# Kernel optimization log

Measured on AMD Instinct MI355X. Metric: run time of the kernel, lower is better.

## Reference

```python
import jax, jax.numpy as jnp
import numpy as np

B, NQ, NK, D_IN, HD = 1, 16384, 7933, 1024, 512
R = 0.3  # keep-top-r fraction used for the quantile threshold


def _l2norm(x):
    # matches F.normalize(p=2, dim=-1, eps=1e-12)
    n = jnp.linalg.norm(x, axis=-1, keepdims=True)
    return x / jnp.maximum(n, 1e-12)


def setup_inputs() -> dict:
    key = jax.random.key(0)
    ks = jax.random.split(key, 10)
    s = 0.02
    return {
        "query": jax.random.normal(ks[0], (B, NQ, D_IN), jnp.float32),
        "key_x": jax.random.normal(ks[1], (B, NK, D_IN), jnp.float32),
        "wq_w": jax.random.normal(ks[2], (HD, D_IN), jnp.float32) * s,
        "wq_b": jnp.zeros((HD,), jnp.float32),
        "wk_w": jax.random.normal(ks[3], (HD, D_IN), jnp.float32) * s,
        "wk_b": jnp.zeros((HD,), jnp.float32),
        "wa_w": jax.random.normal(ks[4], (1, NK), jnp.float32) * s,
        "wa_b": jnp.zeros((1,), jnp.float32),
        "cls_w": jax.random.normal(ks[5], (1, HD), jnp.float32) * s,
        "cls_b": jnp.zeros((1,), jnp.float32),
    }


def reference(query, key_x, wq_w, wq_b, wk_w, wk_b, wa_w, wa_b, cls_w, cls_b):
    # WQ / WK: Linear + Tanh
    q = jnp.tanh(jnp.einsum("bnd,hd->bnh", query, wq_w) + wq_b)   # [B,NQ,HD]
    k = jnp.tanh(jnp.einsum("bnd,hd->bnh", key_x, wk_w) + wk_b)   # [B,NK,HD]
    # normalized dot-product scores
    A = jnp.einsum("bqh,bkh->bqk", _l2norm(q), _l2norm(k))        # [B,NQ,NK]
    # WA: Linear(NK -> 1)
    A1 = jnp.einsum("bqk,ok->bqo", A, wa_w) + wa_b                # [B,NQ,1]
    # quantile threshold from batch 0 (torch: sorted ascending, index -int(r*NQ))
    thre = jax.lax.stop_gradient(jnp.sort(A1[0, :, 0])[-int(R * NQ)])
    A1 = jnp.where(A1 > thre, A1, 0.0)                            # F.threshold(., thre, 0)
    attn = jax.nn.softmax(A1, axis=1)                             # softmax over NQ (zeros included)
    attn_t = jnp.transpose(attn, (0, 2, 1))                       # [B,1,NQ]
    z = jnp.matmul(attn_t, q).reshape(-1, HD)                     # [B,HD]
    y_prob = z @ cls_w.T + cls_b                                  # [B,1]
    return (y_prob, attn_t)
```

## Files before the change

kernel.cpp:

```cpp
#include <hip/hip_runtime.h>
#include <math.h>

#define NQ 16384
#define NK 7933
#define DI 1024
#define HD 512
#define RANK_TARGET 11469

typedef __bf16 bf16x8 __attribute__((ext_vector_type(8)));
typedef float  f32x4  __attribute__((ext_vector_type(4)));

#define GLOAD_LDS16(g, l)                                                     \
  __builtin_amdgcn_global_load_lds(                                           \
      (const __attribute__((address_space(1))) void*)(g),                     \
      (__attribute__((address_space(3))) void*)(l), 16, 0, 0)

__device__ __forceinline__ unsigned mapf(float f) {
  unsigned b = __float_as_uint(f);
  return (b & 0x80000000u) ? ~b : (b | 0x80000000u);
}

__device__ __forceinline__ bf16x8 cvt8(float4 a, float4 b) {
  bf16x8 o;
  o[0] = (__bf16)a.x; o[1] = (__bf16)a.y; o[2] = (__bf16)a.z; o[3] = (__bf16)a.w;
  o[4] = (__bf16)b.x; o[5] = (__bf16)b.y; o[6] = (__bf16)b.z; o[7] = (__bf16)b.w;
  return o;
}

__global__ void conv_wk(const float* __restrict__ wq, const float* __restrict__ wk,
                        const float* __restrict__ key,
                        __bf16* __restrict__ wqbf, __bf16* __restrict__ wkbf,
                        __bf16* __restrict__ kbf, unsigned* __restrict__ zero_region) {
  if (blockIdx.x == 0) {
    for (int j = threadIdx.x; j < 1088; j += 256) zero_region[j] = 0u;
  }
  const int NK8 = NK * DI / 8;
  const int W8  = HD * DI / 8;
  const int total = NK8 + 2 * W8;
  int i = blockIdx.x * blockDim.x + threadIdx.x;
  int stride = gridDim.x * blockDim.x;
  for (; i < total; i += stride) {
    const float* s; __bf16* d; int j;
    if (i < NK8)            { s = key; d = kbf;  j = i; }
    else if (i < NK8 + W8)  { s = wq;  d = wqbf; j = i - NK8; }
    else                    { s = wk;  d = wkbf; j = i - NK8 - W8; }
    float4 a = ((const float4*)s)[2 * j];
    float4 b = ((const float4*)s)[2 * j + 1];
    ((bf16x8*)d)[j] = cvt8(a, b);
  }
}

__global__ __launch_bounds__(512, 4)
void mega_gemms(const __bf16* __restrict__ kbf, const __bf16* __restrict__ wkbf,
                const float* __restrict__ wk_b, const float* __restrict__ wa,
                float* __restrict__ v,
                const float* __restrict__ query, const __bf16* __restrict__ wqbf,
                const float* __restrict__ wq_b, float* __restrict__ qtanh) {
  __shared__ __align__(16) char smem[81920];
  const int bid = blockIdx.x;
  const int tid = threadIdx.x;
  const int lane = tid & 63;
  const int wave = tid >> 6;
  const int srow = lane >> 3;
  const int scol = ((lane & 7) ^ srow) << 3;
  const int lrow = lane & 15;
  const int chi  = lane >> 4;
  constexpr int K = DI;

  if (bid < 124) {
    __bf16* sA = (__bf16*)smem;
    __bf16* sB = (__bf16*)(smem + 16384);
    float* ssrow = (float*)smem;
    const int m0 = bid * 64;

    int gaA = m0 + wave * 8 + srow; if (gaA > NK - 1) gaA = NK - 1;
    const __bf16* Ap = kbf + (size_t)gaA * K + scol;
    const __bf16* Bp[8];
#pragma unroll
    for (int c = 0; c < 8; ++c)
      Bp[c] = wkbf + (size_t)(wave * 64 + c * 8 + srow) * K + scol;

    f32x4 acc[4][4] = {};

    GLOAD_LDS16(Ap, &sA[wave * 512]);
#pragma unroll
    for (int c = 0; c < 8; ++c)
      GLOAD_LDS16(Bp[c], &sB[(wave * 8 + c) * 512]);
    __syncthreads();

    int buf = 0;
    for (int t = 0; t < 16; ++t) {
      const int kk = t * 64;
      if (t < 15)
        GLOAD_LDS16(Ap + kk + 64, &sA[(buf ^ 1) * 4096 + wave * 512]);
      const __bf16* sAc = sA + buf * 4096;
#pragma unroll
      for (int ks = 0; ks < 64; ks += 32) {
        const int cc = (ks >> 3) + chi;
        const int sw = ((cc ^ (lrow & 7)) << 3);
        bf16x8 af[4], bfr[4];
#pragma unroll
        for (int mi = 0; mi < 4; ++mi)
          af[mi] = *(const bf16x8*)(&sAc[(mi * 16 + lrow) * 64 + sw]);
#pragma unroll
        for (int ni = 0; ni < 4; ++ni)
          bfr[ni] = *(const bf16x8*)(&sB[(wave * 64 + ni * 16 + lrow) * 64 + sw]);
#pragma unroll
        for (int mi = 0; mi < 4; ++mi)
#pragma unroll
          for (int ni = 0; ni < 4; ++ni)
            acc[mi][ni] = __builtin_amdgcn_mfma_f32_16x16x32_bf16(af[mi], bfr[ni], acc[mi][ni], 0, 0, 0);
      }
      if (t < 15) {
        __syncthreads();
#pragma unroll
        for (int c = 0; c < 8; ++c)
          GLOAD_LDS16(Bp[c] + kk + 64, &sB[(wave * 8 + c) * 512]);
        __syncthreads();
        buf ^= 1;
      }
    }

    __syncthreads();
    if (tid < 64) ssrow[tid] = 0.f;
    __syncthreads();

    float b4[4];
#pragma unroll
    for (int ni = 0; ni < 4; ++ni) b4[ni] = wk_b[wave * 64 + ni * 16 + lrow];

#pragma unroll
    for (int mi = 0; mi < 4; ++mi)
#pragma unroll
      for (int ni = 0; ni < 4; ++ni)
#pragma unroll
        for (int r = 0; r < 4; ++r)
          acc[mi][ni][r] = tanhf(acc[mi][ni][r] + b4[ni]);

#pragma unroll
    for (int mi = 0; mi < 4; ++mi)
#pragma unroll
      for (int r = 0; r < 4; ++r) {
        float ps = 0.f;
#pragma unroll
        for (int ni = 0; ni < 4; ++ni) ps += acc[mi][ni][r] * acc[mi][ni][r];
#pragma unroll
        for (int off = 1; off < 16; off <<= 1) ps += __shfl_xor(ps, off);
        if ((lane & 15) == 0)
          atomicAdd(&ssrow[mi * 16 + (lane >> 4) * 4 + r], ps);
      }
    __syncthreads();

    if (tid < 64) {
      int grow = m0 + tid;
      float s = 0.f;
      if (grow < NK) s = wa[grow] / fmaxf(sqrtf(ssrow[tid]), 1e-12f);
      ssrow[tid] = s;
    }
    __syncthreads();

    float sc[4][4];
#pragma unroll
    for (int mi = 0; mi < 4; ++mi)
#pragma unroll
      for (int r = 0; r < 4; ++r)
        sc[mi][r] = ssrow[mi * 16 + (lane >> 4) * 4 + r];

#pragma unroll
    for (int ni = 0; ni < 4; ++ni) {
      float cs = 0.f;
#pragma unroll
      for (int mi = 0; mi < 4; ++mi)
#pragma unroll
        for (int r = 0; r < 4; ++r)
          cs += acc[mi][ni][r] * sc[mi][r];
      cs += __shfl_xor(cs, 16);
      cs += __shfl_xor(cs, 32);
      if (lane < 16) atomicAdd(&v[wave * 64 + ni * 16 + lane], cs);
    }
  } else {
    __bf16* sA = (__bf16*)smem;
    __bf16* sB = (__bf16*)(smem + 16384);
    const int qi = bid - 124;
    const int m0 = (qi >> 1) * 64;
    const int n0 = (qi & 1) * 256;
    const int wr = wave >> 2;
    const int wc = wave & 3;

    const int arow = tid >> 3;
    const int acb  = tid & 7;
    const int aoff = arow * 64 + ((acb ^ (arow & 7)) << 3);
    const float* ap = query + (size_t)(m0 + arow) * K + acb * 8;

    const __bf16* Bp0 = wqbf + (size_t)(n0 + (wave * 4 + 0) * 8 + srow) * K + scol;
    const __bf16* Bp1 = wqbf + (size_t)(n0 + (wave * 4 + 1) * 8 + srow) * K + scol;
    const __bf16* Bp2 = wqbf + (size_t)(n0 + (wave * 4 + 2) * 8 + srow) * K + scol;
    const __bf16* Bp3 = wqbf + (size_t)(n0 + (wave * 4 + 3) * 8 + srow) * K + scol;

    f32x4 acc[2][4] = {};

    {
      float4 x0 = *(const float4*)(ap);
      float4 x1 = *(const float4*)(ap + 4);
      GLOAD_LDS16(Bp0, &sB[(wave * 4 + 0) * 512]);
      GLOAD_LDS16(Bp1, &sB[(wave * 4 + 1) * 512]);
      GLOAD_LDS16(Bp2, &sB[(wave * 4 + 2) * 512]);
      GLOAD_LDS16(Bp3, &sB[(wave * 4 + 3) * 512]);
      *(bf16x8*)&sA[aoff] = cvt8(x0, x1);
      __syncthreads();
    }

    int buf = 0;
    for (int t = 0; t < 16; ++t) {
      const int kk = t * 64;
      float4 x0, x1;
      if (t < 15) {
        x0 = *(const float4*)(ap + kk + 64);
        x1 = *(const float4*)(ap + kk + 68);
        const int ob = buf ^ 1;
        GLOAD_LDS16(Bp0 + kk + 64, &sB[ob * 16384 + (wave * 4 + 0) * 512]);
        GLOAD_LDS16(Bp1 + kk + 64, &sB[ob * 16384 + (wave * 4 + 1) * 512]);
        GLOAD_LDS16(Bp2 + kk + 64, &sB[ob * 16384 + (wave * 4 + 2) * 512]);
        GLOAD_LDS16(Bp3 + kk + 64, &sB[ob * 16384 + (wave * 4 + 3) * 512]);
      }
      const __bf16* sAc = sA + buf * 4096;
      const __bf16* sBc = sB + buf * 16384;
#pragma unroll
      for (int ks = 0; ks < 64; ks += 32) {
        const int cc = (ks >> 3) + chi;
        const int sw = ((cc ^ (lrow & 7)) << 3);
        bf16x8 af[2], bfr[4];
        af[0] = *(const bf16x8*)(&sAc[(wr * 32 + lrow) * 64 + sw]);
        af[1] = *(const bf16x8*)(&sAc[(wr * 32 + 16 + lrow) * 64 + sw]);
#pragma unroll
        for (int ni = 0; ni < 4; ++ni)
          bfr[ni] = *(const bf16x8*)(&sBc[(wc * 64 + ni * 16 + lrow) * 64 + sw]);
#pragma unroll
        for (int ni = 0; ni < 4; ++ni) {
          acc[0][ni] = __builtin_amdgcn_mfma_f32_16x16x32_bf16(af[0], bfr[ni], acc[0][ni], 0, 0, 0);
          acc[1][ni] = __builtin_amdgcn_mfma_f32_16x16x32_bf16(af[1], bfr[ni], acc[1][ni], 0, 0, 0);
        }
      }
      if (t < 15) {
        *(bf16x8*)&sA[(buf ^ 1) * 4096 + aoff] = cvt8(x0, x1);
        __syncthreads();
        buf ^= 1;
      }
    }

    const int rbase = m0 + wr * 32 + ((lane >> 4) << 2);
    const int cbase = n0 + wc * 64 + (lane & 15);
    float b4[4];
#pragma unroll
    for (int ni = 0; ni < 4; ++ni) b4[ni] = wq_b[cbase + ni * 16];
#pragma unroll
    for (int mi = 0; mi < 2; ++mi)
#pragma unroll
      for (int r = 0; r < 4; ++r) {
        int grow = rbase + mi * 16 + r;
#pragma unroll
        for (int ni = 0; ni < 4; ++ni)
          qtanh[(size_t)grow * HD + cbase + ni * 16] =
              tanhf(acc[mi][ni][r] + b4[ni]);
      }
  }
}

__global__ __launch_bounds__(256)
void a1_pass(const float* __restrict__ qt, const float* __restrict__ v,
             const float* __restrict__ wa_b, float* __restrict__ A1) {
  const int tid = threadIdx.x, lane = tid & 63, wave = tid >> 6;
  const float wab = wa_b[0];
  const float4* vp = (const float4*)(v + lane * 8);
  float4 vv0 = vp[0], vv1 = vp[1];
  const int gw = blockIdx.x * 4 + wave;
  for (int r = gw; r < NQ; r += 2048) {
    const float4* p = (const float4*)(qt + (size_t)r * HD + lane * 8);
    float4 u = p[0], w = p[1];
    float dot = u.x * vv0.x + u.y * vv0.y + u.z * vv0.z + u.w * vv0.w
              + w.x * vv1.x + w.y * vv1.y + w.z * vv1.z + w.w * vv1.w;
    float ss  = u.x * u.x + u.y * u.y + u.z * u.z + u.w * u.w
              + w.x * w.x + w.y * w.y + w.z * w.z + w.w * w.w;
#pragma unroll
    for (int off = 32; off; off >>= 1) {
      dot += __shfl_xor(dot, off);
      ss  += __shfl_xor(ss, off);
    }
    if (lane == 0) A1[r] = dot / fmaxf(sqrtf(ss), 1e-12f) + wab;
  }
}

__global__ __launch_bounds__(1024)
void select_kernel(const float* __restrict__ A1, float* __restrict__ scf) {
  __shared__ unsigned wred1[16], wred2[16], wred3[16];
  __shared__ unsigned s_res;
  const int t = threadIdx.x, lane = t & 63, wave = t >> 6;
  unsigned kloc[16];
#pragma unroll 4
  for (int j = 0; j < 16; ++j) kloc[j] = mapf(A1[j * 1024 + t]);
  if (t == 0) s_res = 0u;
  __syncthreads();

  for (int b = 30; b >= 0; b -= 2) {
    const unsigned res = s_res;
    const unsigned t1 = res | (1u << b);
    const unsigned t2 = res | (2u << b);
    const unsigned t3 = res | (3u << b);
    unsigned c1 = 0, c2 = 0, c3 = 0;
#pragma unroll
    for (int j = 0; j < 16; ++j) {
      unsigned k = kloc[j];
      c1 += (k < t1); c2 += (k < t2); c3 += (k < t3);
    }
#pragma unroll
    for (int off = 32; off; off >>= 1) {
      c1 += __shfl_xor(c1, off);
      c2 += __shfl_xor(c2, off);
      c3 += __shfl_xor(c3, off);
    }
    if (lane == 0) { wred1[wave] = c1; wred2[wave] = c2; wred3[wave] = c3; }
    __syncthreads();
    if (t == 0) {
      unsigned C1 = 0, C2 = 0, C3 = 0;
      for (int w = 0; w < 16; ++w) { C1 += wred1[w]; C2 += wred2[w]; C3 += wred3[w]; }
      unsigned nr = res;
      if (C3 <= RANK_TARGET)      nr = t3;
      else if (C2 <= RANK_TARGET) nr = t2;
      else if (C1 <= RANK_TARGET) nr = t1;
      s_res = nr;
    }
    __syncthreads();
  }
  if (t == 0) {
    unsigned key = s_res;
    unsigned bits = (key & 0x80000000u) ? (key ^ 0x80000000u) : ~key;
    scf[0] = __uint_as_float(bits);
  }
}

__global__ __launch_bounds__(256)
void expz(const float* __restrict__ A1, const float* __restrict__ qt,
          float* __restrict__ scf, float* __restrict__ e_out,
          float* __restrict__ z) {
  __shared__ float vpart[4][512];
  __shared__ float esum[4];
  const int tid = threadIdx.x, lane = tid & 63, wave = tid >> 6;
  const float thre = scf[0];
  const int gw = blockIdx.x * 4 + wave;
  const int tw = gridDim.x * 4;
  float acc[8] = {0, 0, 0, 0, 0, 0, 0, 0};
  float es = 0.f;
  for (int r = gw; r < NQ; r += tw) {
    float x = A1[r]; x = (x > thre) ? x : 0.f;
    float e = expf(x - thre);
    if (lane == 0) e_out[r] = e;
    es += e;
    const float4* p = (const float4*)(qt + (size_t)r * HD + lane * 8);
    float4 u = p[0], w = p[1];
    acc[0] += e * u.x; acc[1] += e * u.y; acc[2] += e * u.z; acc[3] += e * u.w;
    acc[4] += e * w.x; acc[5] += e * w.y; acc[6] += e * w.z; acc[7] += e * w.w;
  }
  if (lane == 0) esum[wave] = es;
#pragma unroll
  for (int j = 0; j < 8; ++j) vpart[wave][lane * 8 + j] = acc[j];
  __syncthreads();
  for (int c = tid; c < 512; c += 256)
    atomicAdd(&z[c], vpart[0][c] + vpart[1][c] + vpart[2][c] + vpart[3][c]);
  if (tid == 0) atomicAdd(&scf[2], esum[0] + esum[1] + esum[2] + esum[3]);
}

__global__ __launch_bounds__(256)
void finalize(float* __restrict__ attn, const float* __restrict__ scf,
              const float* __restrict__ z, const float* __restrict__ cls_w,
              const float* __restrict__ cls_b, float* __restrict__ y) {
  const float invZ = 1.f / scf[2];
  if (blockIdx.x < 64) {
    int i = blockIdx.x * 256 + threadIdx.x;
    attn[i] *= invZ;
  } else if (threadIdx.x < 64) {
    const int lane = threadIdx.x;
    const float4* zp = (const float4*)(z + lane * 8);
    const float4* wp = (const float4*)(cls_w + lane * 8);
    float4 a = zp[0], b = zp[1], c = wp[0], d = wp[1];
    float dot = a.x * c.x + a.y * c.y + a.z * c.z + a.w * c.w
              + b.x * d.x + b.y * d.y + b.z * d.z + b.w * d.w;
#pragma unroll
    for (int off = 32; off; off >>= 1) dot += __shfl_xor(dot, off);
    if (lane == 0) y[0] = dot * invZ + cls_b[0];
  }
}

#define OFF_WQBF 0u
#define OFF_WKBF 1048576u
#define OFF_KBF  2097152u
#define OFF_QT   18874368u
#define OFF_A1   52428800u
#define OFF_V    52494336u
#define OFF_Z    52496384u
#define OFF_SC   52498432u

extern "C" void kernel_launch(void* const* d_in, const int* in_sizes, int n_in,
                              void* d_out, int out_size, void* d_ws, size_t ws_size,
                              hipStream_t stream) {
  const float* query = (const float*)d_in[0];
  const float* key_x = (const float*)d_in[1];
  const float* wq_w  = (const float*)d_in[2];
  const float* wq_b  = (const float*)d_in[3];
  const float* wk_w  = (const float*)d_in[4];
  const float* wk_b  = (const float*)d_in[5];
  const float* wa_w  = (const float*)d_in[6];
  const float* wa_b  = (const float*)d_in[7];
  const float* cls_w = (const float*)d_in[8];
  const float* cls_b = (const float*)d_in[9];
  float* out = (float*)d_out;

  char* ws = (char*)d_ws;
  __bf16* wqbf  = (__bf16*)(ws + OFF_WQBF);
  __bf16* wkbf  = (__bf16*)(ws + OFF_WKBF);
  __bf16* kbf   = (__bf16*)(ws + OFF_KBF);
  float*  qtanh = (float*)(ws + OFF_QT);
  float*  A1    = (float*)(ws + OFF_A1);
  float*  v     = (float*)(ws + OFF_V);
  float*  z     = (float*)(ws + OFF_Z);
  float*  scf   = (float*)(ws + OFF_SC);
  float*  out_attn = out + 1;

  conv_wk<<<2048, 256, 0, stream>>>(wq_w, wk_w, key_x, wqbf, wkbf, kbf,
                                    (unsigned*)v);

  mega_gemms<<<636, 512, 0, stream>>>(kbf, wkbf, wk_b, wa_w, v,
                                      query, wqbf, wq_b, qtanh);

  a1_pass<<<512, 256, 0, stream>>>(qtanh, v, wa_b, A1);

  select_kernel<<<1, 1024, 0, stream>>>(A1, scf);

  expz<<<256, 256, 0, stream>>>(A1, qtanh, scf, out_attn, z);

  finalize<<<65, 256, 0, stream>>>(out_attn, scf, z, cls_w, cls_b, out);
}
```

Before: 243.8 us.

## Fuse tail kernels via last-block atomics and double-buffer both WK GEMM operands

Merges a1_pass with the single-block select kernel, and expz with finalize. Each merged kernel uses an atomic completion counter so the last block to finish runs the serial tail, removing two kernel launches. The K-projection GEMM branch also changes to 32-wide K steps with both A and B double-buffered in LDS, dropping the extra mid-loop barrier that the single-buffered B tile needed. The counters cnt1/cnt2 are never reset in the code shown and must be zeroed before every call (possibly by conv_wk), otherwise the last-block check fails.

```diff
diff --git a/kernel.cpp b/kernel.cpp
--- a/kernel.cpp
+++ b/kernel.cpp
@@ -61,61 +61,64 @@
   const int tid = threadIdx.x;
   const int lane = tid & 63;
   const int wave = tid >> 6;
-  const int srow = lane >> 3;
-  const int scol = ((lane & 7) ^ srow) << 3;
   const int lrow = lane & 15;
   const int chi  = lane >> 4;
   constexpr int K = DI;
 
   if (bid < 124) {
     __bf16* sA = (__bf16*)smem;
-    __bf16* sB = (__bf16*)(smem + 16384);
+    __bf16* sB = (__bf16*)(smem + 8192);
     float* ssrow = (float*)smem;
     const int m0 = bid * 64;
 
-    int gaA = m0 + wave * 8 + srow; if (gaA > NK - 1) gaA = NK - 1;
-    const __bf16* Ap = kbf + (size_t)gaA * K + scol;
-    const __bf16* Bp[8];
-#pragma unroll
-    for (int c = 0; c < 8; ++c)
-      Bp[c] = wkbf + (size_t)(wave * 64 + c * 8 + srow) * K + scol;
+    const int srow2 = lane >> 2;
+    const int scol2 = ((lane & 3) ^ ((lane >> 3) & 3)) << 3;
+
+    const int aseg = wave & 3;
+    int garow = m0 + aseg * 16 + srow2; if (garow > NK - 1) garow = NK - 1;
+    const __bf16* Ap = kbf + (size_t)garow * K + scol2;
+    const __bf16* Bp[4];
+#pragma unroll
+    for (int c = 0; c < 4; ++c)
+      Bp[c] = wkbf + (size_t)((wave * 4 + c) * 16 + srow2) * K + scol2;
 
     f32x4 acc[4][4] = {};
 
-    GLOAD_LDS16(Ap, &sA[wave * 512]);
-#pragma unroll
-    for (int c = 0; c < 8; ++c)
-      GLOAD_LDS16(Bp[c], &sB[(wave * 8 + c) * 512]);
+    if (wave < 4) GLOAD_LDS16(Ap, &sA[aseg * 512]);
+#pragma unroll
+    for (int c = 0; c < 4; ++c)
+      GLOAD_LDS16(Bp[c], &sB[(wave * 4 + c) * 512]);
     __syncthreads();
 
     int buf = 0;
-    for (int t = 0; t < 16; ++t) {
-      const int kk = t * 64;
-      if (t < 15)
-        GLOAD_LDS16(Ap + kk + 64, &sA[(buf ^ 1) * 4096 + wave * 512]);
-      const __bf16* sAc = sA + buf * 4096;
-#pragma unroll
-      for (int ks = 0; ks < 64; ks += 32) {
-        const int cc = (ks >> 3) + chi;
-        const int sw = ((cc ^ (lrow & 7)) << 3);
-        bf16x8 af[4], bfr[4];
-#pragma unroll
-        for (int mi = 0; mi < 4; ++mi)
-          af[mi] = *(const bf16x8*)(&sAc[(mi * 16 + lrow) * 64 + sw]);
+    for (int t = 0; t < 32; ++t) {
+      const int kk = t * 32;
+      if (t < 31) {
+        const int ob = buf ^ 1;
+        if (wave < 4) GLOAD_LDS16(Ap + kk + 32, &sA[ob * 2048 + aseg * 512]);
+#pragma unroll
+        for (int c = 0; c < 4; ++c)
+          GLOAD_LDS16(Bp[c] + kk + 32, &sB[ob * 16384 + (wave * 4 + c) * 512]);
+      }
+      const __bf16* sAc = sA + buf * 2048;
+      const __bf16* sBc = sB + buf * 16384;
+      bf16x8 af[4], bfr[4];
+#pragma unroll
+      for (int mi = 0; mi < 4; ++mi) {
+        const int row = mi * 16 + lrow;
+        af[mi] = *(const bf16x8*)(&sAc[row * 32 + ((chi ^ ((row >> 1) & 3)) << 3)]);
+      }
+#pragma unroll
+      for (int ni = 0; ni < 4; ++ni) {
+        const int row = wave * 64 + ni * 16 + lrow;
+        bfr[ni] = *(const bf16x8*)(&sBc[row * 32 + ((chi ^ ((row >> 1) & 3)) << 3)]);
+      }
+#pragma unroll
+      for (int mi = 0; mi < 4; ++mi)
 #pragma unroll
         for (int ni = 0; ni < 4; ++ni)
-          bfr[ni] = *(const bf16x8*)(&sB[(wave * 64 + ni * 16 + lrow) * 64 + sw]);
-#pragma unroll
-        for (int mi = 0; mi < 4; ++mi)
-#pragma unroll
-          for (int ni = 0; ni < 4; ++ni)
-            acc[mi][ni] = __builtin_amdgcn_mfma_f32_16x16x32_bf16(af[mi], bfr[ni], acc[mi][ni], 0, 0, 0);
-      }
-      if (t < 15) {
-        __syncthreads();
-#pragma unroll
-        for (int c = 0; c < 8; ++c)
-          GLOAD_LDS16(Bp[c] + kk + 64, &sB[(wave * 8 + c) * 512]);
+          acc[mi][ni] = __builtin_amdgcn_mfma_f32_16x16x32_bf16(af[mi], bfr[ni], acc[mi][ni], 0, 0, 0);
+      if (t < 31) {
         __syncthreads();
         buf ^= 1;
       }
@@ -179,6 +182,8 @@
       if (lane < 16) atomicAdd(&v[wave * 64 + ni * 16 + lane], cs);
     }
   } else {
+    const int srow = lane >> 3;
+    const int scol = ((lane & 7) ^ srow) << 3;
     __bf16* sA = (__bf16*)smem;
     __bf16* sB = (__bf16*)(smem + 16384);
     const int qi = bid - 124;
@@ -266,14 +271,18 @@
   }
 }
 
-__global__ __launch_bounds__(256)
-void a1_pass(const float* __restrict__ qt, const float* __restrict__ v,
-             const float* __restrict__ wa_b, float* __restrict__ A1) {
+__global__ __launch_bounds__(1024)
+void a1_select(const float* __restrict__ qt, const float* __restrict__ v,
+               const float* __restrict__ wa_b, float* __restrict__ A1,
+               float* __restrict__ scf, unsigned* __restrict__ cnt) {
+  __shared__ unsigned wred1[16], wred2[16], wred3[16];
+  __shared__ unsigned s_res;
+  __shared__ unsigned s_t;
   const int tid = threadIdx.x, lane = tid & 63, wave = tid >> 6;
   const float wab = wa_b[0];
   const float4* vp = (const float4*)(v + lane * 8);
   float4 vv0 = vp[0], vv1 = vp[1];
-  const int gw = blockIdx.x * 4 + wave;
+  const int gw = blockIdx.x * 16 + wave;
   for (int r = gw; r < NQ; r += 2048) {
     const float4* p = (const float4*)(qt + (size_t)r * HD + lane * 8);
     float4 u = p[0], w = p[1];
@@ -288,17 +297,19 @@
     }
     if (lane == 0) A1[r] = dot / fmaxf(sqrtf(ss), 1e-12f) + wab;
   }
-}
-
-__global__ __launch_bounds__(1024)
-void select_kernel(const float* __restrict__ A1, float* __restrict__ scf) {
-  __shared__ unsigned wred1[16], wred2[16], wred3[16];
-  __shared__ unsigned s_res;
-  const int t = threadIdx.x, lane = t & 63, wave = t >> 6;
+
+  __threadfence();
+  __syncthreads();
+  if (tid == 0) s_t = atomicAdd(cnt, 1u);
+  __syncthreads();
+  if (s_t != 127) return;
+  __threadfence();
+
+  volatile const float* A1v = A1;
   unsigned kloc[16];
 #pragma unroll 4
-  for (int j = 0; j < 16; ++j) kloc[j] = mapf(A1[j * 1024 + t]);
-  if (t == 0) s_res = 0u;
+  for (int j = 0; j < 16; ++j) kloc[j] = mapf(A1v[j * 1024 + tid]);
+  if (tid == 0) s_res = 0u;
   __syncthreads();
 
   for (int b = 30; b >= 0; b -= 2) {
@@ -320,7 +331,7 @@
     }
     if (lane == 0) { wred1[wave] = c1; wred2[wave] = c2; wred3[wave] = c3; }
     __syncthreads();
-    if (t == 0) {
+    if (tid == 0) {
       unsigned C1 = 0, C2 = 0, C3 = 0;
       for (int w = 0; w < 16; ++w) { C1 += wred1[w]; C2 += wred2[w]; C3 += wred3[w]; }
       unsigned nr = res;
@@ -331,7 +342,7 @@
     }
     __syncthreads();
   }
-  if (t == 0) {
+  if (tid == 0) {
     unsigned key = s_res;
     unsigned bits = (key & 0x80000000u) ? (key ^ 0x80000000u) : ~key;
     scf[0] = __uint_as_float(bits);
@@ -339,15 +350,18 @@
 }
 
 __global__ __launch_bounds__(256)
-void expz(const float* __restrict__ A1, const float* __restrict__ qt,
-          float* __restrict__ scf, float* __restrict__ e_out,
-          float* __restrict__ z) {
+void expz_fin(const float* __restrict__ A1, const float* __restrict__ qt,
+              float* __restrict__ scf, float* __restrict__ e_out,
+              float* __restrict__ z, const float* __restrict__ cls_w,
+              const float* __restrict__ cls_b, float* __restrict__ y,
+              unsigned* __restrict__ cnt) {
   __shared__ float vpart[4][512];
   __shared__ float esum[4];
+  __shared__ unsigned s_t;
   const int tid = threadIdx.x, lane = tid & 63, wave = tid >> 6;
   const float thre = scf[0];
   const int gw = blockIdx.x * 4 + wave;
-  const int tw = gridDim.x * 4;
+  const int tw = 256 * 4;
   float acc[8] = {0, 0, 0, 0, 0, 0, 0, 0};
   float es = 0.f;
   for (int r = gw; r < NQ; r += tw) {
@@ -367,26 +381,27 @@
   for (int c = tid; c < 512; c += 256)
     atomicAdd(&z[c], vpart[0][c] + vpart[1][c] + vpart[2][c] + vpart[3][c]);
   if (tid == 0) atomicAdd(&scf[2], esum[0] + esum[1] + esum[2] + esum[3]);
-}
-
-__global__ __launch_bounds__(256)
-void finalize(float* __restrict__ attn, const float* __restrict__ scf,
-              const float* __restrict__ z, const float* __restrict__ cls_w,
-              const float* __restrict__ cls_b, float* __restrict__ y) {
-  const float invZ = 1.f / scf[2];
-  if (blockIdx.x < 64) {
-    int i = blockIdx.x * 256 + threadIdx.x;
-    attn[i] *= invZ;
-  } else if (threadIdx.x < 64) {
-    const int lane = threadIdx.x;
-    const float4* zp = (const float4*)(z + lane * 8);
-    const float4* wp = (const float4*)(cls_w + lane * 8);
-    float4 a = zp[0], b = zp[1], c = wp[0], d = wp[1];
-    float dot = a.x * c.x + a.y * c.y + a.z * c.z + a.w * c.w
-              + b.x * d.x + b.y * d.y + b.z * d.z + b.w * d.w;
+
+  __threadfence();
+  __syncthreads();
+  if (tid == 0) s_t = atomicAdd(cnt, 1u);
+  __syncthreads();
+  if (s_t != 255) return;
+  __threadfence();
+
+  const float S = *(volatile float*)&scf[2];
+  const float invZ = 1.f / S;
+  volatile const float* ev = e_out;
+  for (int i = tid; i < NQ; i += 256) e_out[i] = ev[i] * invZ;
+  if (tid < 64) {
+    volatile const float* zv = z;
+    float dot = 0.f;
+#pragma unroll
+    for (int j = 0; j < 8; ++j)
+      dot += zv[tid * 8 + j] * cls_w[tid * 8 + j];
 #pragma unroll
     for (int off = 32; off; off >>= 1) dot += __shfl_xor(dot, off);
-    if (lane == 0) y[0] = dot * invZ + cls_b[0];
+    if (tid == 0) y[0] = dot * invZ + cls_b[0];
   }
 }
 
@@ -423,6 +438,8 @@
   float*  v     = (float*)(ws + OFF_V);
   float*  z     = (float*)(ws + OFF_Z);
   float*  scf   = (float*)(ws + OFF_SC);
+  unsigned* cnt1 = (unsigned*)(scf + 8);
+  unsigned* cnt2 = (unsigned*)(scf + 9);
   float*  out_attn = out + 1;
 
   conv_wk<<<2048, 256, 0, stream>>>(wq_w, wk_w, key_x, wqbf, wkbf, kbf,
@@ -431,11 +448,8 @@
   mega_gemms<<<636, 512, 0, stream>>>(kbf, wkbf, wk_b, wa_w, v,
                                       query, wqbf, wq_b, qtanh);
 
-  a1_pass<<<512, 256, 0, stream>>>(qtanh, v, wa_b, A1);
-
-  select_kernel<<<1, 1024, 0, stream>>>(A1, scf);
-
-  expz<<<256, 256, 0, stream>>>(A1, qtanh, scf, out_attn, z);
-
-  finalize<<<65, 256, 0, stream>>>(out_attn, scf, z, cls_w, cls_b, out);
-}
+  a1_select<<<128, 1024, 0, stream>>>(qtanh, v, wa_b, A1, scf, cnt1);
+
+  expz_fin<<<256, 256, 0, stream>>>(A1, qtanh, scf, out_attn, z,
+                                    cls_w, cls_b, out, cnt2);
+}
```

Result: slower. 314.8 us (+29.1%).
